# Kernel tuning notes

Measured on AMD Instinct MI355X. Metric: run time of the kernel, lower is better.

## Reference

```python
import jax, jax.numpy as jnp
import numpy as np

D_MODEL = 1024
NUM_HEADS = 16
HEAD_DIM = D_MODEL // NUM_HEADS
WINDOW = 16
DILATION = 3
SCALE = HEAD_DIM ** -0.5


def _linear(x, W, b):
    # torch nn.Linear: y = x @ W.T + b, W: [out, in]
    return x @ W.T + b


def _chunk_attention(x, Wq, bq, Wk, bk, Wv, bv, chunk):
    B, L, D = x.shape
    pad = (-L) % chunk
    if pad:
        x = jnp.pad(x, ((0, 0), (0, pad), (0, 0)))
    Lp = L + pad
    nC = Lp // chunk
    xr = x.reshape(B * nC, chunk, D)  # [BC, c, D]

    def heads(t):
        return t.reshape(B * nC, chunk, NUM_HEADS, HEAD_DIM).transpose(0, 2, 1, 3)

    q = heads(_linear(xr, Wq, bq))  # [BC, H, c, hd]
    k = heads(_linear(xr, Wk, bk))
    v = heads(_linear(xr, Wv, bv))
    attn = jax.nn.softmax(jnp.einsum('bhqd,bhkd->bhqk', q, k) * SCALE, axis=-1)
    out = jnp.einsum('bhqk,bhkd->bhqd', attn, v)  # [BC, H, c, hd]
    out = out.transpose(0, 2, 1, 3).reshape(B, Lp, D)
    return out[:, :L, :]


def setup_inputs() -> dict:
    key = jax.random.key(0)
    ks = jax.random.split(key, 9)
    s = 1.0 / np.sqrt(D_MODEL)
    x = jax.random.normal(ks[0], (4, 4096, D_MODEL), dtype=jnp.float32)
    def lin(kw, kb):
        W = jax.random.uniform(kw, (D_MODEL, D_MODEL), minval=-s, maxval=s, dtype=jnp.float32)
        b = jax.random.uniform(kb, (D_MODEL,), minval=-s, maxval=s, dtype=jnp.float32)
        return W, b
    Wq, bq = lin(ks[1], ks[2])
    Wk, bk = lin(ks[3], ks[4])
    Wv, bv = lin(ks[5], ks[6])
    Wo, bo = lin(ks[7], ks[8])
    return {"x": x, "Wq": Wq, "bq": bq, "Wk": Wk, "bk": bk,
            "Wv": Wv, "bv": bv, "Wo": Wo, "bo": bo}


def reference(x, Wq, bq, Wk, bk, Wv, bv, Wo, bo):
    B, L, D = x.shape
    # local windowed attention
    local_out = _chunk_attention(x, Wq, bq, Wk, bk, Wv, bv, WINDOW)
    # dilated (atrous) attention: stride-DILATION interleave via reshape/permute
    pad = (-L) % DILATION
    x_pad = jnp.pad(x, ((0, 0), (0, pad), (0, 0))) if pad else x
    Lp = L + pad
    xv = x_pad.reshape(B, Lp // DILATION, DILATION, D).transpose(0, 2, 1, 3)
    x_atrous = xv.reshape(B * DILATION, Lp // DILATION, D)
    a = _chunk_attention(x_atrous, Wq, bq, Wk, bk, Wv, bv, WINDOW)
    a = a.reshape(B, DILATION, Lp // DILATION, D).transpose(0, 2, 1, 3).reshape(B, Lp, D)
    atrous_out = a[:, :L, :]
    return _linear(local_out + atrous_out, Wo, bo)
```

## Files before the change

### kernel.cpp

```cpp
#include <hip/hip_runtime.h>
#include <hip/hip_bf16.h>
#include <stdint.h>

typedef unsigned short ushort_t;
typedef __attribute__((ext_vector_type(8))) short bf16x8;
typedef __attribute__((ext_vector_type(4))) float f32x4;

__device__ __forceinline__ ushort_t f2bf(float f) {
    uint32_t u = __builtin_bit_cast(uint32_t, f);
    u += 0x7FFF + ((u >> 16) & 1);
    return (ushort_t)(u >> 16);
}
__device__ __forceinline__ float bf2f(ushort_t h) {
    return __builtin_bit_cast(float, (uint32_t)h << 16);
}

__device__ __forceinline__ f32x4 mfma16(bf16x8 a, bf16x8 b, f32x4 c) {
    return __builtin_amdgcn_mfma_f32_16x16x32_bf16(a, b, c, 0, 0, 0);
}

#define GLL(g, l) __builtin_amdgcn_global_load_lds(                              \
    (const __attribute__((address_space(1))) void*)(g),                          \
    (__attribute__((address_space(3))) void*)(l), 16, 0, 0)

#define CFENCE asm volatile("" ::: "memory")
#define BARRIER do { CFENCE; __builtin_amdgcn_s_barrier(); CFENCE; } while (0)


__device__ __forceinline__ void cvt8(const float* s, ushort_t* d) {
    float4 a = ((const float4*)s)[0], b = ((const float4*)s)[1];
    union { bf16x8 v; ushort_t u[8]; } o;
    o.u[0] = f2bf(a.x); o.u[1] = f2bf(a.y); o.u[2] = f2bf(a.z); o.u[3] = f2bf(a.w);
    o.u[4] = f2bf(b.x); o.u[5] = f2bf(b.y); o.u[6] = f2bf(b.z); o.u[7] = f2bf(b.w);
    *(bf16x8*)d = o.v;
}

__global__ __launch_bounds__(256) void cvt_all(
    const float* __restrict__ x,
    const float* __restrict__ Wq, const float* __restrict__ Wk,
    const float* __restrict__ Wv, const float* __restrict__ Wo,
    const float* __restrict__ bq, const float* __restrict__ bk,
    const float* __restrict__ bv,
    ushort_t* __restrict__ xb, ushort_t* __restrict__ wqkv,
    float* __restrict__ bqkv)
{
    const int NX = 16384 * 1024 / 8;
    const int NW = 1024 * 1024 / 8;
    int i = blockIdx.x * 256 + threadIdx.x;
    if (i < NX) {
        cvt8(x + (size_t)i * 8, xb + (size_t)i * 8);
    } else if (i < NX + 4 * NW) {
        int j = i - NX;
        int w = j >> 17, off = j & (NW - 1);
        const float* s = (w == 0) ? Wq : (w == 1) ? Wk : (w == 2) ? Wv : Wo;
        cvt8(s + (size_t)off * 8, wqkv + (size_t)j * 8);
    } else if (i < NX + 4 * NW + 384) {
        int j = i - NX - 4 * NW;
        int w2 = j >> 7, off = j & 127;
        const float* s = (w2 == 0) ? bq : (w2 == 1) ? bk : bv;
        ((float4*)(bqkv + j * 8))[0] = ((const float4*)(s + off * 8))[0];
        ((float4*)(bqkv + j * 8))[1] = ((const float4*)(s + off * 8))[1];
    }
}


#define STAGE_A(jj)  { int idx = (jj) * 512 + tid; int row = idx >> 3, ch = idx & 7;    \
    GLL(A + (size_t)(m0 + row) * 1024 + kt2 * 64 + ((ch ^ (row & 7)) * 8),             \
        (char*)Abn + (size_t)idx * 16); }
#define STAGE_B(jj)  { int idx = (jj) * 512 + tid; int row = idx >> 3, ch = idx & 7;    \
    GLL(B + (size_t)(n0 + row) * 1024 + kt2 * 64 + ((ch ^ (row & 7)) * 8),             \
        (char*)Bbn + (size_t)idx * 16); }

template<int MODE>
__global__ __launch_bounds__(512, 2) void gemm3(
    const ushort_t* __restrict__ A, const ushort_t* __restrict__ B,
    const float* __restrict__ bias, void* __restrict__ outp,
    int M, int NTN)
{
    __shared__ ushort_t As[3][256 * 64];
    __shared__ ushort_t Bs[3][128 * 64];
    const int NK = 16;

    const int nwg = gridDim.x;
    const int bid = blockIdx.x;
    const int q8 = nwg >> 3;
    const int swz = (bid & 7) * q8 + (bid >> 3);
    const int m0 = (swz / NTN) * 256;
    const int n0 = (swz % NTN) * 128;

    const int tid = threadIdx.x;
    const int wave = tid >> 6, lane = tid & 63;
    const int wm = wave >> 1, wn = wave & 1;
    const int lg = lane >> 4, ln = lane & 15;

    f32x4 acc[4][4];
#pragma unroll
    for (int i = 0; i < 4; ++i)
#pragma unroll
        for (int j = 0; j < 4; ++j) acc[i][j] = (f32x4){0.f, 0.f, 0.f, 0.f};

    {
        ushort_t* Abn = &As[0][0]; ushort_t* Bbn = &Bs[0][0]; int kt2 = 0;
        STAGE_A(0) STAGE_A(1) STAGE_A(2) STAGE_A(3) STAGE_B(0) STAGE_B(1)
    }
    {
        ushort_t* Abn = &As[1][0]; ushort_t* Bbn = &Bs[1][0]; int kt2 = 1;
        STAGE_A(0) STAGE_A(1) STAGE_A(2) STAGE_A(3) STAGE_B(0) STAGE_B(1)
    }
    asm volatile("s_waitcnt vmcnt(6)" ::: "memory");
    BARRIER;

    int bc = 0;
    for (int kt = 0; kt < NK; ++kt) {
        int bn = bc + 2; if (bn >= 3) bn -= 3;
        const ushort_t* Ab = &As[bc][0];
        const ushort_t* Bb = &Bs[bc][0];
        ushort_t* Abn = &As[bn][0];
        ushort_t* Bbn = &Bs[bn][0];
        const int kt2 = kt + 2;
        const bool pf = (kt2 < NK);

        bf16x8 af[4][2], b01[2][2];
#pragma unroll
        for (int mi = 0; mi < 4; ++mi) {
            int row = wm * 64 + mi * 16 + ln;
#pragma unroll
            for (int kk = 0; kk < 2; ++kk)
                af[mi][kk] = *(const bf16x8*)&Ab[row * 64 + (((kk * 4 + lg) ^ (row & 7)) * 8)];
        }
#pragma unroll
        for (int ni = 0; ni < 2; ++ni) {
            int row = wn * 64 + ni * 16 + ln;
#pragma unroll
            for (int kk = 0; kk < 2; ++kk)
                b01[ni][kk] = *(const bf16x8*)&Bb[row * 64 + (((kk * 4 + lg) ^ (row & 7)) * 8)];
        }
        if (pf) { STAGE_A(0) STAGE_A(1) STAGE_A(2) }
        BARRIER;
        __builtin_amdgcn_s_setprio(1);
#pragma unroll
        for (int mi = 0; mi < 4; ++mi)
#pragma unroll
            for (int ni = 0; ni < 2; ++ni) {
                acc[mi][ni] = mfma16(af[mi][0], b01[ni][0], acc[mi][ni]);
                acc[mi][ni] = mfma16(af[mi][1], b01[ni][1], acc[mi][ni]);
            }
        __builtin_amdgcn_s_setprio(0);

        bf16x8 b23[2][2];
#pragma unroll
        for (int ni = 0; ni < 2; ++ni) {
            int row = wn * 64 + (ni + 2) * 16 + ln;
#pragma unroll
            for (int kk = 0; kk < 2; ++kk)
                b23[ni][kk] = *(const bf16x8*)&Bb[row * 64 + (((kk * 4 + lg) ^ (row & 7)) * 8)];
        }
        if (pf) { STAGE_A(3) STAGE_B(0) STAGE_B(1) }
        BARRIER;
        __builtin_amdgcn_s_setprio(1);
#pragma unroll
        for (int mi = 0; mi < 4; ++mi)
#pragma unroll
            for (int ni = 0; ni < 2; ++ni) {
                acc[mi][ni + 2] = mfma16(af[mi][0], b23[ni][0], acc[mi][ni + 2]);
                acc[mi][ni + 2] = mfma16(af[mi][1], b23[ni][1], acc[mi][ni + 2]);
            }
        __builtin_amdgcn_s_setprio(0);

        if (pf) { asm volatile("s_waitcnt vmcnt(6)" ::: "memory"); }
        else    { asm volatile("s_waitcnt vmcnt(0)" ::: "memory"); }
        BARRIER;
        bc += 1; if (bc == 3) bc = 0;
    }

#pragma unroll
    for (int ni = 0; ni < 4; ++ni) {
        int n = n0 + wn * 64 + ni * 16 + ln;
        float bval = bias[n];
#pragma unroll
        for (int mi = 0; mi < 4; ++mi) {
#pragma unroll
            for (int r = 0; r < 4; ++r) {
                int m = m0 + wm * 64 + mi * 16 + lg * 4 + r;
                float v = acc[mi][ni][r] + bval;
                if (MODE == 0) {
                    int which = n >> 10, col = n & 1023;
                    ((ushort_t*)outp)[(size_t)which * ((size_t)M * 1024)
                                      + (size_t)m * 1024 + col] = f2bf(v);
                } else {
                    ((float*)outp)[(size_t)m * 1024 + n] = v;
                }
            }
        }
    }
}


__device__ __forceinline__ bf16x8 bias8(const float* __restrict__ b, int off) {
    float4 f0 = *(const float4*)(b + off);
    float4 f1 = *(const float4*)(b + off + 4);
    union { bf16x8 v; ushort_t u[8]; } o;
    o.u[0] = f2bf(f0.x); o.u[1] = f2bf(f0.y); o.u[2] = f2bf(f0.z); o.u[3] = f2bf(f0.w);
    o.u[4] = f2bf(f1.x); o.u[5] = f2bf(f1.y); o.u[6] = f2bf(f1.z); o.u[7] = f2bf(f1.w);
    return o.v;
}


__global__ __launch_bounds__(256) void attn_local(
    const ushort_t* __restrict__ Q, const ushort_t* __restrict__ K,
    const ushort_t* __restrict__ V, ushort_t* __restrict__ S)
{
    const int wave = threadIdx.x >> 6, lane = threadIdx.x & 63;
    const int unit = blockIdx.x * 4 + wave;
    const int h = unit & 15;
    const int c = unit >> 4;
    const int g = lane >> 4, nn = lane & 15;
    __shared__ ushort_t lds_p[4][16 * 16];
    __shared__ ushort_t vt[4][64 * 16];

    const size_t rowb = (size_t)c * 16;
    size_t aoff = (rowb + nn) * 1024 + h * 64 + g * 8;
    bf16x8 qa0 = *(const bf16x8*)(Q + aoff);
    bf16x8 qa1 = *(const bf16x8*)(Q + aoff + 32);
    bf16x8 kb0 = *(const bf16x8*)(K + aoff);
    bf16x8 kb1 = *(const bf16x8*)(K + aoff + 32);
    f32x4 sc = {0.f, 0.f, 0.f, 0.f};
    sc = mfma16(qa0, kb0, sc);
    sc = mfma16(qa1, kb1, sc);

#pragma unroll
    for (int r = 0; r < 4; ++r) {
        float s = sc[r] * 0.125f;
        float mx = s;
#pragma unroll
        for (int off = 1; off < 16; off <<= 1) mx = fmaxf(mx, __shfl_xor(mx, off, 64));
        float e = __expf(s - mx);
        float sm = e;
#pragma unroll
        for (int off = 1; off < 16; off <<= 1) sm += __shfl_xor(sm, off, 64);
        lds_p[wave][(g * 4 + r) * 16 + nn] = f2bf(e / sm);
    }

#pragma unroll
    for (int it = 0; it < 2; ++it) {
        int u = it * 64 + lane;
        int n = u >> 3, cc = u & 7;
        bf16x8 vv = *(const bf16x8*)(V + (rowb + n) * 1024 + h * 64 + cc * 8);
        union { bf16x8 v; ushort_t u8[8]; } vu; vu.v = vv;
#pragma unroll
        for (int j = 0; j < 8; ++j) vt[wave][(cc * 8 + j) * 16 + n] = vu.u8[j];
    }
    __syncthreads();

    bf16x8 zero8 = {};
    bf16x8 pa = (g < 2) ? *(const bf16x8*)&lds_p[wave][nn * 16 + g * 8] : zero8;
#pragma unroll
    for (int dt = 0; dt < 4; ++dt) {
        bf16x8 vb = (g < 2) ? *(const bf16x8*)&vt[wave][(dt * 16 + nn) * 16 + g * 8] : zero8;
        f32x4 o = mfma16(pa, vb, (f32x4){0.f, 0.f, 0.f, 0.f});
#pragma unroll
        for (int r = 0; r < 4; ++r) {
            size_t orow = rowb + g * 4 + r;
            S[orow * 1024 + h * 64 + dt * 16 + nn] = f2bf(o[r]);
        }
    }
}


__global__ __launch_bounds__(256) void attn_atrous(
    const ushort_t* __restrict__ Q, const ushort_t* __restrict__ K,
    const ushort_t* __restrict__ V,
    const float* __restrict__ bq, const float* __restrict__ bk,
    const float* __restrict__ bv, ushort_t* __restrict__ S)
{
    const int wave = threadIdx.x >> 6, lane = threadIdx.x & 63;
    const int unit = blockIdx.x * 4 + wave;
    const int h = unit & 15;
    const int tmp = unit >> 4;
    const int c = tmp % 86;
    const int sidx = tmp / 86;
    const int b = sidx / 3, dil = sidx % 3;
    const int g = lane >> 4, nn = lane & 15;
    __shared__ ushort_t lds_p[4][16 * 16];
    __shared__ ushort_t vt[4][64 * 16];

    const int dof = h * 64 + g * 8;
    const int p_n = 3 * (c * 16 + nn) + dil;
    bf16x8 qa0, qa1, kb0, kb1;
    if (p_n < 4096) {
        size_t o = ((size_t)b * 4096 + p_n) * 1024 + dof;
        qa0 = *(const bf16x8*)(Q + o);
        qa1 = *(const bf16x8*)(Q + o + 32);
        kb0 = *(const bf16x8*)(K + o);
        kb1 = *(const bf16x8*)(K + o + 32);
    } else {
        qa0 = bias8(bq, dof); qa1 = bias8(bq, dof + 32);
        kb0 = bias8(bk, dof); kb1 = bias8(bk, dof + 32);
    }
    f32x4 sc = {0.f, 0.f, 0.f, 0.f};
    sc = mfma16(qa0, kb0, sc);
    sc = mfma16(qa1, kb1, sc);

#pragma unroll
    for (int r = 0; r < 4; ++r) {
        float s = sc[r] * 0.125f;
        float mx = s;
#pragma unroll
        for (int off = 1; off < 16; off <<= 1) mx = fmaxf(mx, __shfl_xor(mx, off, 64));
        float e = __expf(s - mx);
        float sm = e;
#pragma unroll
        for (int off = 1; off < 16; off <<= 1) sm += __shfl_xor(sm, off, 64);
        lds_p[wave][(g * 4 + r) * 16 + nn] = f2bf(e / sm);
    }

#pragma unroll
    for (int it = 0; it < 2; ++it) {
        int u = it * 64 + lane;
        int n = u >> 3, cc = u & 7;
        int p_v = 3 * (c * 16 + n) + dil;
        bf16x8 vv = (p_v < 4096)
            ? *(const bf16x8*)(V + ((size_t)b * 4096 + p_v) * 1024 + h * 64 + cc * 8)
            : bias8(bv, h * 64 + cc * 8);
        union { bf16x8 v; ushort_t u8[8]; } vu; vu.v = vv;
#pragma unroll
        for (int j = 0; j < 8; ++j) vt[wave][(cc * 8 + j) * 16 + n] = vu.u8[j];
    }
    __syncthreads();

    bf16x8 zero8 = {};
    bf16x8 pa = (g < 2) ? *(const bf16x8*)&lds_p[wave][nn * 16 + g * 8] : zero8;
#pragma unroll
    for (int dt = 0; dt < 4; ++dt) {
        bf16x8 vb = (g < 2) ? *(const bf16x8*)&vt[wave][(dt * 16 + nn) * 16 + g * 8] : zero8;
        f32x4 o = mfma16(pa, vb, (f32x4){0.f, 0.f, 0.f, 0.f});
#pragma unroll
        for (int r = 0; r < 4; ++r) {
            int p_q = 3 * (c * 16 + g * 4 + r) + dil;
            if (p_q < 4096) {
                size_t off = ((size_t)b * 4096 + p_q) * 1024 + h * 64 + dt * 16 + nn;
                S[off] = f2bf(bf2f(S[off]) + o[r]);
            }
        }
    }
}


extern "C" void kernel_launch(void* const* d_in, const int* in_sizes, int n_in,
                              void* d_out, int out_size, void* d_ws, size_t ws_size,
                              hipStream_t stream)
{
    const float* x  = (const float*)d_in[0];
    const float* Wq = (const float*)d_in[1];
    const float* bq = (const float*)d_in[2];
    const float* Wk = (const float*)d_in[3];
    const float* bk = (const float*)d_in[4];
    const float* Wv = (const float*)d_in[5];
    const float* bv = (const float*)d_in[6];
    const float* Wo = (const float*)d_in[7];
    const float* bo = (const float*)d_in[8];
    float* out = (float*)d_out;

    const size_t NT = 16384;
    ushort_t* xb   = (ushort_t*)d_ws;
    ushort_t* wqkv = xb + NT * 1024;
    ushort_t* wo   = wqkv + 3 * 1024 * 1024;
    ushort_t* Qb   = wo + 1024 * 1024;
    ushort_t* Kb   = Qb + NT * 1024;
    ushort_t* Vb   = Kb + NT * 1024;
    ushort_t* Sb   = Vb + NT * 1024;
    float*    bqkv = (float*)(Sb + NT * 1024);

    const int total_units = 2097152 + 4 * 131072 + 384;
    cvt_all<<<(total_units + 255) / 256, 256, 0, stream>>>(
        x, Wq, Wk, Wv, Wo, bq, bk, bv, xb, wqkv, bqkv);

    gemm3<0><<<1536, 512, 0, stream>>>(xb, wqkv, bqkv, (void*)Qb, (int)NT, 24);

    attn_local <<<4096, 256, 0, stream>>>(Qb, Kb, Vb, Sb);
    attn_atrous<<<4128, 256, 0, stream>>>(Qb, Kb, Vb, bq, bk, bv, Sb);

    gemm3<1><<<512, 512, 0, stream>>>(Sb, wo, bo, (void*)out, (int)NT, 8);
}
```

Baseline: 368.4 us.

## Enlarge GEMM tiles to 256x256 with an eight-phase interleaved load/MFMA pipeline

Replaces the 256x128-tile triple-buffered GEMM with a 256x256 tile per workgroup. Each wave now computes a 128x64 sub-tile, and the k-loop is split into eight phases that interleave half-tile global-to-LDS loads with MFMA quadrants, using priority changes and scheduling barriers. The larger tile raises arithmetic intensity and halves the grid for both the QKV and output projections. In exchange it doubles the accumulator registers (possible spilling at two waves per SIMD), adds more barriers, and leaves fewer workgroups per CU to balance the load, especially for the 256-block output GEMM.

```diff
diff --git a/kernel.cpp b/kernel.cpp
--- a/kernel.cpp
+++ b/kernel.cpp
@@ -25,6 +25,11 @@
 
 #define CFENCE asm volatile("" ::: "memory")
 #define BARRIER do { CFENCE; __builtin_amdgcn_s_barrier(); CFENCE; } while (0)
+#define PRIO1 __builtin_amdgcn_s_setprio(1)
+#define PRIO0 __builtin_amdgcn_s_setprio(0)
+#define PH_SYNC do { BARRIER;                                                    \
+    asm volatile("s_waitcnt lgkmcnt(0)" ::: "memory");                           \
+    __builtin_amdgcn_sched_barrier(0); } while (0)
 
 
 __device__ __forceinline__ void cvt8(const float* s, ushort_t* d) {
@@ -64,113 +69,124 @@
 }
 
 
-#define STAGE_A(jj)  { int idx = (jj) * 512 + tid; int row = idx >> 3, ch = idx & 7;    \
-    GLL(A + (size_t)(m0 + row) * 1024 + kt2 * 64 + ((ch ^ (row & 7)) * 8),             \
-        (char*)Abn + (size_t)idx * 16); }
-#define STAGE_B(jj)  { int idx = (jj) * 512 + tid; int row = idx >> 3, ch = idx & 7;    \
-    GLL(B + (size_t)(n0 + row) * 1024 + kt2 * 64 + ((ch ^ (row & 7)) * 8),             \
-        (char*)Bbn + (size_t)idx * 16); }
+#define STG(P, rb, slot, h, kt) {                                                \
+    _Pragma("unroll")                                                            \
+    for (int j = 0; j < 2; ++j) {                                                \
+        int idx = j * 512 + tid; int row = idx >> 3, ch = idx & 7;               \
+        GLL(P + (size_t)((rb) + (h) * 128 + row) * 1024 + (kt) * 64              \
+              + ((ch ^ (row & 7)) * 8),                                          \
+            (char*)(slot) + (size_t)idx * 16);                                   \
+    } }
+
+#define LDA4(d, mibase)                                                          \
+    _Pragma("unroll")                                                            \
+    for (int q = 0; q < 4; ++q)                                                  \
+        _Pragma("unroll")                                                        \
+        for (int kk = 0; kk < 2; ++kk)                                           \
+            a[q][kk] = *(const bf16x8*)&As[(d) * 2 + wm]                         \
+                [((mibase) + q) * 1024 + ln * 64 + cho[kk]];
+
+#define LDB2(d, nibase)                                                          \
+    _Pragma("unroll")                                                            \
+    for (int q = 0; q < 2; ++q)                                                  \
+        _Pragma("unroll")                                                        \
+        for (int kk = 0; kk < 2; ++kk)                                           \
+            bfr[(nibase) + q][kk] = *(const bf16x8*)&Bs[(d) * 2 + bh]            \
+                [brow0 + ((nibase) + q) * 1024 + ln * 64 + cho[kk]];
+
+#define MFMA_Q(qm, qn)                                                           \
+    _Pragma("unroll")                                                            \
+    for (int mi = 0; mi < 4; ++mi)                                               \
+        _Pragma("unroll")                                                        \
+        for (int nl = 0; nl < 2; ++nl) {                                         \
+            acc[(qm)*4+mi][(qn)*2+nl] =                                          \
+                mfma16(a[mi][0], bfr[(qn)*2+nl][0], acc[(qm)*4+mi][(qn)*2+nl]);  \
+            acc[(qm)*4+mi][(qn)*2+nl] =                                          \
+                mfma16(a[mi][1], bfr[(qn)*2+nl][1], acc[(qm)*4+mi][(qn)*2+nl]);  \
+        }
 
 template<int MODE>
-__global__ __launch_bounds__(512, 2) void gemm3(
+__global__ __launch_bounds__(512, 2) void gemm8(
     const ushort_t* __restrict__ A, const ushort_t* __restrict__ B,
     const float* __restrict__ bias, void* __restrict__ outp,
     int M, int NTN)
 {
-    __shared__ ushort_t As[3][256 * 64];
-    __shared__ ushort_t Bs[3][128 * 64];
-    const int NK = 16;
-
+    __shared__ ushort_t As[4][128 * 64];
+    __shared__ ushort_t Bs[4][128 * 64];
+
+    const int bid = blockIdx.x;
     const int nwg = gridDim.x;
-    const int bid = blockIdx.x;
     const int q8 = nwg >> 3;
     const int swz = (bid & 7) * q8 + (bid >> 3);
     const int m0 = (swz / NTN) * 256;
-    const int n0 = (swz % NTN) * 128;
+    const int n0 = (swz % NTN) * 256;
 
     const int tid = threadIdx.x;
     const int wave = tid >> 6, lane = tid & 63;
-    const int wm = wave >> 1, wn = wave & 1;
+    const int wm = wave >> 2, wn = wave & 3;
     const int lg = lane >> 4, ln = lane & 15;
-
-    f32x4 acc[4][4];
-#pragma unroll
-    for (int i = 0; i < 4; ++i)
-#pragma unroll
-        for (int j = 0; j < 4; ++j) acc[i][j] = (f32x4){0.f, 0.f, 0.f, 0.f};
-
-    {
-        ushort_t* Abn = &As[0][0]; ushort_t* Bbn = &Bs[0][0]; int kt2 = 0;
-        STAGE_A(0) STAGE_A(1) STAGE_A(2) STAGE_A(3) STAGE_B(0) STAGE_B(1)
-    }
-    {
-        ushort_t* Abn = &As[1][0]; ushort_t* Bbn = &Bs[1][0]; int kt2 = 1;
-        STAGE_A(0) STAGE_A(1) STAGE_A(2) STAGE_A(3) STAGE_B(0) STAGE_B(1)
-    }
-    asm volatile("s_waitcnt vmcnt(6)" ::: "memory");
+    const int bh = wn >> 1;
+    const int brow0 = (wn & 1) * 4096;
+    int cho[2];
+    cho[0] = ((0 * 4 + lg) ^ (ln & 7)) * 8;
+    cho[1] = ((1 * 4 + lg) ^ (ln & 7)) * 8;
+
+    f32x4 acc[8][4];
+#pragma unroll
+    for (int i2 = 0; i2 < 8; ++i2)
+#pragma unroll
+        for (int j2 = 0; j2 < 4; ++j2) acc[i2][j2] = (f32x4){0.f, 0.f, 0.f, 0.f};
+
+    STG(A, m0, &As[0][0], 0, 0)
+    STG(A, m0, &As[1][0], 1, 0)
+    STG(B, n0, &Bs[0][0], 0, 0)
+    STG(B, n0, &Bs[1][0], 1, 0)
+    STG(B, n0, &Bs[2][0], 0, 1)
+    STG(B, n0, &Bs[3][0], 1, 1)
+    asm volatile("s_waitcnt vmcnt(4)" ::: "memory");
     BARRIER;
 
-    int bc = 0;
-    for (int kt = 0; kt < NK; ++kt) {
-        int bn = bc + 2; if (bn >= 3) bn -= 3;
-        const ushort_t* Ab = &As[bc][0];
-        const ushort_t* Bb = &Bs[bc][0];
-        ushort_t* Abn = &As[bn][0];
-        ushort_t* Bbn = &Bs[bn][0];
-        const int kt2 = kt + 2;
-        const bool pf = (kt2 < NK);
-
-        bf16x8 af[4][2], b01[2][2];
-#pragma unroll
-        for (int mi = 0; mi < 4; ++mi) {
-            int row = wm * 64 + mi * 16 + ln;
-#pragma unroll
-            for (int kk = 0; kk < 2; ++kk)
-                af[mi][kk] = *(const bf16x8*)&Ab[row * 64 + (((kk * 4 + lg) ^ (row & 7)) * 8)];
-        }
-#pragma unroll
-        for (int ni = 0; ni < 2; ++ni) {
-            int row = wn * 64 + ni * 16 + ln;
-#pragma unroll
-            for (int kk = 0; kk < 2; ++kk)
-                b01[ni][kk] = *(const bf16x8*)&Bb[row * 64 + (((kk * 4 + lg) ^ (row & 7)) * 8)];
-        }
-        if (pf) { STAGE_A(0) STAGE_A(1) STAGE_A(2) }
-        BARRIER;
-        __builtin_amdgcn_s_setprio(1);
-#pragma unroll
-        for (int mi = 0; mi < 4; ++mi)
-#pragma unroll
-            for (int ni = 0; ni < 2; ++ni) {
-                acc[mi][ni] = mfma16(af[mi][0], b01[ni][0], acc[mi][ni]);
-                acc[mi][ni] = mfma16(af[mi][1], b01[ni][1], acc[mi][ni]);
-            }
-        __builtin_amdgcn_s_setprio(0);
-
-        bf16x8 b23[2][2];
-#pragma unroll
-        for (int ni = 0; ni < 2; ++ni) {
-            int row = wn * 64 + (ni + 2) * 16 + ln;
-#pragma unroll
-            for (int kk = 0; kk < 2; ++kk)
-                b23[ni][kk] = *(const bf16x8*)&Bb[row * 64 + (((kk * 4 + lg) ^ (row & 7)) * 8)];
-        }
-        if (pf) { STAGE_A(3) STAGE_B(0) STAGE_B(1) }
-        BARRIER;
-        __builtin_amdgcn_s_setprio(1);
-#pragma unroll
-        for (int mi = 0; mi < 4; ++mi)
-#pragma unroll
-            for (int ni = 0; ni < 2; ++ni) {
-                acc[mi][ni + 2] = mfma16(af[mi][0], b23[ni][0], acc[mi][ni + 2]);
-                acc[mi][ni + 2] = mfma16(af[mi][1], b23[ni][1], acc[mi][ni + 2]);
-            }
-        __builtin_amdgcn_s_setprio(0);
-
-        if (pf) { asm volatile("s_waitcnt vmcnt(6)" ::: "memory"); }
+    for (int i = 0; i < 8; ++i) {
+        const int kA1 = 2 * i + 1;
+        const int kN  = 2 * i + 2;
+        const int kN1 = 2 * i + 3;
+        const bool pf = (i < 7);
+        bf16x8 a[4][2], bfr[4][2];
+
+        LDA4(0, 0) LDB2(0, 0)
+        STG(A, m0, &As[2][0], 0, kA1)
+        PH_SYNC; PRIO1; MFMA_Q(0, 0) PRIO0;
+        BARRIER;
+        LDB2(0, 2)
+        STG(A, m0, &As[3][0], 1, kA1)
+        PH_SYNC; PRIO1; MFMA_Q(0, 1) PRIO0;
+        BARRIER;
+        LDA4(0, 4)
+        if (pf) STG(B, n0, &Bs[0][0], 0, kN)
+        PH_SYNC; PRIO1; MFMA_Q(1, 0) PRIO0;
+        BARRIER;
+        if (pf) STG(B, n0, &Bs[1][0], 1, kN)
+        PRIO1; MFMA_Q(1, 1) PRIO0;
+        if (pf) { asm volatile("s_waitcnt vmcnt(4)" ::: "memory"); }
         else    { asm volatile("s_waitcnt vmcnt(0)" ::: "memory"); }
         BARRIER;
-        bc += 1; if (bc == 3) bc = 0;
+        LDA4(1, 0) LDB2(1, 0)
+        if (pf) STG(A, m0, &As[0][0], 0, kN)
+        PH_SYNC; PRIO1; MFMA_Q(0, 0) PRIO0;
+        BARRIER;
+        LDB2(1, 2)
+        if (pf) STG(A, m0, &As[1][0], 1, kN)
+        PH_SYNC; PRIO1; MFMA_Q(0, 1) PRIO0;
+        BARRIER;
+        LDA4(1, 4)
+        if (pf) STG(B, n0, &Bs[2][0], 0, kN1)
+        PH_SYNC; PRIO1; MFMA_Q(1, 0) PRIO0;
+        BARRIER;
+        if (pf) STG(B, n0, &Bs[3][0], 1, kN1)
+        PRIO1; MFMA_Q(1, 1) PRIO0;
+        if (pf) { asm volatile("s_waitcnt vmcnt(4)" ::: "memory"); }
+        else    { asm volatile("s_waitcnt vmcnt(0)" ::: "memory"); }
+        BARRIER;
     }
 
 #pragma unroll
@@ -178,10 +194,10 @@
         int n = n0 + wn * 64 + ni * 16 + ln;
         float bval = bias[n];
 #pragma unroll
-        for (int mi = 0; mi < 4; ++mi) {
+        for (int mi = 0; mi < 8; ++mi) {
 #pragma unroll
             for (int r = 0; r < 4; ++r) {
-                int m = m0 + wm * 64 + mi * 16 + lg * 4 + r;
+                int m = m0 + wm * 128 + mi * 16 + lg * 4 + r;
                 float v = acc[mi][ni][r] + bval;
                 if (MODE == 0) {
                     int which = n >> 10, col = n & 1023;
@@ -375,10 +391,10 @@
     cvt_all<<<(total_units + 255) / 256, 256, 0, stream>>>(
         x, Wq, Wk, Wv, Wo, bq, bk, bv, xb, wqkv, bqkv);
 
-    gemm3<0><<<1536, 512, 0, stream>>>(xb, wqkv, bqkv, (void*)Qb, (int)NT, 24);
+    gemm8<0><<<768, 512, 0, stream>>>(xb, wqkv, bqkv, (void*)Qb, (int)NT, 12);
 
     attn_local <<<4096, 256, 0, stream>>>(Qb, Kb, Vb, Sb);
     attn_atrous<<<4128, 256, 0, stream>>>(Qb, Kb, Vb, bq, bk, bv, Sb);
 
-    gemm3<1><<<512, 512, 0, stream>>>(Sb, wo, bo, (void*)out, (int)NT, 8);
-}
+    gemm8<1><<<256, 512, 0, stream>>>(Sb, wo, bo, (void*)out, (int)NT, 4);
+}
```

After: 378.3 us. 1.03x slower.
